# Kernel tuning notes

Measured on AMD Instinct MI355X. Metric: run time of the kernel, lower is better.

The kernel has to match this reference:

```python
import jax, jax.numpy as jnp
import numpy as np

BN_EPS = 1e-5
BN_SCALE = 1.0 / np.sqrt(1.0 + BN_EPS).astype(np.float32)  # running_mean=0, running_var=1


def _conv1x1(x, w, b=None):
    y = jnp.einsum('bchw,oc->bohw', x, w)
    if b is not None:
        y = y + b.reshape(1, -1, 1, 1)
    return y


def _bn(x, g, b):
    # eval-mode BN with running_mean=0, running_var=1
    return x * (BN_SCALE * g).reshape(1, -1, 1, 1) + b.reshape(1, -1, 1, 1)


def _spatial_attn(x, w, b):
    avg = jnp.mean(x, axis=1, keepdims=True)
    mx = jnp.max(x, axis=1, keepdims=True)
    s = jnp.concatenate([avg, mx], axis=1)  # [B,2,H,W]
    y = jax.lax.conv_general_dilated(s, w, (1, 1), [(3, 3), (3, 3)],
                                     dimension_numbers=('NCHW', 'OIHW', 'NCHW'))
    return jax.nn.sigmoid(y + b.reshape(1, -1, 1, 1))  # [B,1,H,W]


def _channel_attn(x, w1, b1, w2, b2):
    avg = jnp.mean(x, axis=(2, 3))  # [B,C]
    mx = jnp.max(x, axis=(2, 3))
    fc = lambda v: jax.nn.relu(v @ w1.T + b1) @ w2.T + b2
    return jax.nn.sigmoid(fc(avg) + fc(mx))[:, :, None, None]  # [B,C,1,1]


def setup_inputs() -> dict:
    key = jax.random.key(0)
    B, C, H, W = 8, 256, 48, 48
    Cr, Cm = C // 8, C // 16
    ks = iter(jax.random.split(key, 24))
    n = lambda shape, scale=0.05: jax.random.normal(next(ks), shape, jnp.float32) * scale
    return dict(
        rgb=jax.random.normal(next(ks), (B, C, H, W), jnp.float32),
        chm=jax.random.normal(next(ks), (B, C, H, W), jnp.float32),
        rgb_sa_w=n((1, 2, 7, 7)), rgb_sa_b=jnp.zeros((1,), jnp.float32),
        chm_sa_w=n((1, 2, 7, 7)), chm_sa_b=jnp.zeros((1,), jnp.float32),
        rgb_fc1_w=n((Cm, C)), rgb_fc1_b=jnp.zeros((Cm,), jnp.float32),
        rgb_fc2_w=n((C, Cm)), rgb_fc2_b=jnp.zeros((C,), jnp.float32),
        chm_fc1_w=n((Cm, C)), chm_fc1_b=jnp.zeros((Cm,), jnp.float32),
        chm_fc2_w=n((C, Cm)), chm_fc2_b=jnp.zeros((C,), jnp.float32),
        rq_w=n((Cr, C)), rq_b=jnp.zeros((Cr,), jnp.float32),
        rk_w=n((Cr, C)), rk_b=jnp.zeros((Cr,), jnp.float32),
        rv_w=n((C, C)), rv_b=jnp.zeros((C,), jnp.float32),
        dq_w=n((Cr, C)), dq_b=jnp.zeros((Cr,), jnp.float32),
        dk_w=n((Cr, C)), dk_b=jnp.zeros((Cr,), jnp.float32),
        dv_w=n((C, C)), dv_b=jnp.zeros((C,), jnp.float32),
        gate_w=n((C, 2 * C)), gate_b=jnp.zeros((C,), jnp.float32),
        mlp1_w=n((24, C)), mlp1_g=jnp.ones((24,), jnp.float32), mlp1_b=jnp.zeros((24,), jnp.float32),
        mlp2_w=n((1, 24)), mlp2_g=jnp.ones((1,), jnp.float32), mlp2_b=jnp.zeros((1,), jnp.float32),
    )


def reference(rgb, chm, rgb_sa_w, rgb_sa_b, chm_sa_w, chm_sa_b,
              rgb_fc1_w, rgb_fc1_b, rgb_fc2_w, rgb_fc2_b,
              chm_fc1_w, chm_fc1_b, chm_fc2_w, chm_fc2_b,
              rq_w, rq_b, rk_w, rk_b, rv_w, rv_b,
              dq_w, dq_b, dk_w, dk_b, dv_w, dv_b,
              gate_w, gate_b, mlp1_w, mlp1_g, mlp1_b, mlp2_w, mlp2_g, mlp2_b):
    B, C, H, W = rgb.shape
    N = H * W
    Cr = rq_w.shape[0]
    scale = Cr ** -0.5

    # channel / spatial attentions
    rgb_sa = _spatial_attn(rgb, rgb_sa_w, rgb_sa_b)
    chm_sa = _spatial_attn(chm, chm_sa_w, chm_sa_b)
    rgb_ca = _channel_attn(rgb, rgb_fc1_w, rgb_fc1_b, rgb_fc2_w, rgb_fc2_b)
    chm_ca = _channel_attn(chm, chm_fc1_w, chm_fc1_b, chm_fc2_w, chm_fc2_b)

    attn_rgb = rgb * chm_sa * chm_ca
    attn_chm = chm * rgb_sa * rgb_ca

    # CAWF dual cross-modal attention
    flat = lambda x: x.reshape(B, -1, N)
    rq = flat(_conv1x1(rgb, rq_w, rq_b))   # [B,Cr,N]
    rk = flat(_conv1x1(rgb, rk_w, rk_b))
    rv = flat(_conv1x1(rgb, rv_w, rv_b))   # [B,C,N]
    dq = flat(_conv1x1(chm, dq_w, dq_b))
    dk = flat(_conv1x1(chm, dk_w, dk_b))
    dv = flat(_conv1x1(chm, dv_w, dv_b))

    rgb_attn = jax.nn.softmax(jnp.einsum('bcn,bcm->bnm', rq, dk) * scale, axis=-1)  # [B,N,N]
    chm_attn = jax.nn.softmax(jnp.einsum('bcn,bcm->bnm', dq, rk) * scale, axis=-1)
    rgb_att = jnp.einsum('bcn,bnm->bcm', rv, rgb_attn).reshape(B, C, H, W)
    chm_att = jnp.einsum('bcn,bnm->bcm', dv, chm_attn).reshape(B, C, H, W)

    c = jnp.concatenate([rgb_att, chm_att], axis=1)
    g = jax.nn.sigmoid(_conv1x1(c, gate_w, gate_b))
    c_fused = rgb_att * g + chm_att * (1.0 - g)
    d_fused = rgb_att * chm_att
    output = c_fused + d_fused

    h = jax.nn.relu(_bn(_conv1x1(output, mlp1_w), mlp1_g, mlp1_b))
    h = jax.nn.sigmoid(_bn(_conv1x1(h, mlp2_w), mlp2_g, mlp2_b))
    weight = jax.nn.sigmoid(h)  # double sigmoid as in original mlp (ConvBNSig + nn.Sigmoid)

    return attn_rgb + attn_chm * weight
```

## Files before the change

### kernel.cpp

```cpp
#include <hip/hip_runtime.h>
#include <hip/hip_bf16.h>
#include <cstdint>

#define DI __device__ __forceinline__

typedef float f32x4 __attribute__((ext_vector_type(4)));
typedef short bf16x8 __attribute__((ext_vector_type(8)));
typedef unsigned short u16x4 __attribute__((ext_vector_type(4)));

constexpr int B_ = 8, C_ = 256, HH = 48, WW = 48, N_ = 2304, CR = 32;
constexpr float QK_SCALE = 0.17677669529663687f;
constexpr float BN_SC = 0.99999500003749968f;

constexpr size_t QK_SZ   = (size_t)B_*N_*CR*2;
constexpr size_t V_SZ    = (size_t)B_*C_*N_*2;
constexpr size_t OFF_RQT = 0;
constexpr size_t OFF_RKT = OFF_RQT + QK_SZ;
constexpr size_t OFF_DQT = OFF_RKT + QK_SZ;
constexpr size_t OFF_DKT = OFF_DQT + QK_SZ;
constexpr size_t OFF_RV  = OFF_DKT + QK_SZ;
constexpr size_t OFF_DV  = OFF_RV + V_SZ;
constexpr size_t OFF_ATT = OFF_DV + V_SZ;
constexpr size_t ATT_SZ  = 2ull*B_*C_*N_*2;
constexpr size_t OFF_FUSED = OFF_RV;
constexpr size_t OFF_SCONV = OFF_ATT + ATT_SZ;
constexpr size_t SCONV_SZ  = 2ull*B_*2*N_*4;
constexpr size_t OFF_SA    = OFF_SCONV + SCONV_SZ;
constexpr size_t SA_SZ     = 2ull*B_*N_*4;
constexpr size_t OFF_CAVG  = OFF_SA + SA_SZ;
constexpr size_t CST_SZ    = 2ull*B_*C_*4;
constexpr size_t OFF_CMAX  = OFF_CAVG + CST_SZ;
constexpr size_t OFF_CA    = OFF_CMAX + CST_SZ;
constexpr size_t OFF_WMAP  = OFF_CA + CST_SZ;
constexpr size_t OFF_WPROJ = OFF_WMAP + (size_t)B_*N_*4;
constexpr size_t WPROJ_SZ  = 2ull*320*256*2;
constexpr size_t OFF_WGATE = OFF_WPROJ + WPROJ_SZ;
constexpr size_t WS_NEEDED = OFF_WGATE + 256ull*512*2;

DI float bf2f(unsigned short u){ union{unsigned int i; float f;} v; v.i = ((unsigned int)u)<<16; return v.f; }
DI unsigned short f2bf(float f){ union{float f; unsigned int i;} v; v.f=f; unsigned int r = v.i + 0x7fffu + ((v.i>>16)&1u); return (unsigned short)(r>>16); }
DI float sigm(float x){ return 1.0f/(1.0f+__expf(-x)); }
DI u16x4 pk4(float p0, float p1, float p2, float p3){
  union { __hip_bfloat162 h[2]; u16x4 v; } u;
  u.h[0] = __float22bfloat162_rn(make_float2(p0, p1));
  u.h[1] = __float22bfloat162_rn(make_float2(p2, p3));
  return u.v;
}

__global__ void k_prep_w(const float* rq_w, const float* rk_w, const float* rv_w,
                         const float* dq_w, const float* dk_w, const float* dv_w,
                         const float* gate_w, unsigned short* wproj, unsigned short* wgate){
  int i = blockIdx.x*256 + threadIdx.x;
  if (i < 163840){
    int mod = i / 81920, r = (i >> 8) % 320, c = i & 255;
    const float* q = mod ? dq_w : rq_w;
    const float* k = mod ? dk_w : rk_w;
    const float* v = mod ? dv_w : rv_w;
    float val = (r < 32) ? q[r*256+c] : (r < 64 ? k[(r-32)*256+c] : v[(r-64)*256+c]);
    wproj[i] = f2bf(val);
  } else {
    int j = i - 163840;
    if (j < 131072) wgate[j] = f2bf(gate_w[j]);
  }
}

__global__ void k_red_spatial(const float* rgb, const float* chm, float* sconv){
  int mod = blockIdx.y;
  const float* X = mod ? chm : rgb;
  int b = blockIdx.x / (N_/64);
  int pix0 = (blockIdx.x % (N_/64)) * 64;
  int p = threadIdx.x & 63, g = threadIdx.x >> 6;
  const float* base = X + (size_t)b*C_*N_ + pix0 + p;
  float s = 0.f, mx = -INFINITY;
  for (int c = g*64; c < g*64+64; ++c){ float v = base[(size_t)c*N_]; s += v; mx = fmaxf(mx, v); }
  __shared__ float ls[4][64], lm[4][64];
  ls[g][p] = s; lm[g][p] = mx;
  __syncthreads();
  if (g == 0){
    s = ls[0][p]+ls[1][p]+ls[2][p]+ls[3][p];
    mx = fmaxf(fmaxf(lm[0][p],lm[1][p]), fmaxf(lm[2][p],lm[3][p]));
    sconv[((size_t)(mod*B_+b)*2 + 0)*N_ + pix0+p] = s*(1.f/256.f);
    sconv[((size_t)(mod*B_+b)*2 + 1)*N_ + pix0+p] = mx;
  }
}

__global__ void k_red_channel(const float* rgb, const float* chm, float* cavg, float* cmax){
  int mod = blockIdx.y;
  const float* X = mod ? chm : rgb;
  int b = blockIdx.x >> 8, c = blockIdx.x & 255;
  const float* base = X + ((size_t)b*C_ + c)*N_;
  float s = 0.f, mx = -INFINITY;
  for (int i = threadIdx.x; i < N_; i += 256){ float v = base[i]; s += v; mx = fmaxf(mx, v); }
  for (int m = 32; m; m >>= 1){ s += __shfl_xor(s, m); mx = fmaxf(mx, __shfl_xor(mx, m)); }
  __shared__ float ss[4], sm[4];
  int w = threadIdx.x >> 6;
  if ((threadIdx.x & 63) == 0){ ss[w] = s; sm[w] = mx; }
  __syncthreads();
  if (threadIdx.x == 0){
    s = ss[0]+ss[1]+ss[2]+ss[3];
    mx = fmaxf(fmaxf(sm[0],sm[1]), fmaxf(sm[2],sm[3]));
    cavg[(mod*B_+b)*C_ + c] = s*(1.f/(float)N_);
    cmax[(mod*B_+b)*C_ + c] = mx;
  }
}

__global__ void k_sa_ca(const float* sconv, const float* rgb_sa_w, const float* rgb_sa_b,
                        const float* chm_sa_w, const float* chm_sa_b, float* sa,
                        const float* cavg, const float* cmax,
                        const float* rw1, const float* rb1, const float* rw2, const float* rb2,
                        const float* cw1, const float* cb1, const float* cw2, const float* cb2,
                        float* ca){
  int x = blockIdx.x;
  if (x < 144){
    int mod = x / 72;
    int idx = (x % 72)*256 + threadIdx.x;
    int b = idx / N_, pix = idx % N_;
    int y = pix / WW, xx0 = pix % WW;
    const float* w7 = mod ? chm_sa_w : rgb_sa_w;
    float acc = (mod ? chm_sa_b : rgb_sa_b)[0];
    const float* sin0 = sconv + (size_t)(mod*B_+b)*2*N_;
    #pragma unroll
    for (int ic = 0; ic < 2; ++ic)
      for (int ky = 0; ky < 7; ++ky){
        int yy = y + ky - 3; if (yy < 0 || yy >= HH) continue;
        for (int kx = 0; kx < 7; ++kx){
          int xx = xx0 + kx - 3; if (xx < 0 || xx >= WW) continue;
          acc += w7[(ic*7+ky)*7+kx] * sin0[ic*N_ + yy*WW + xx];
        }
      }
    sa[(mod*B_+b)*N_ + pix] = sigm(acc);
  } else {
    int y = x - 144;
    int mod = y >> 3, b = y & 7;
    const float* w1 = mod ? cw1 : rw1;  const float* b1 = mod ? cb1 : rb1;
    const float* w2 = mod ? cw2 : rw2;  const float* b2 = mod ? cb2 : rb2;
    __shared__ float va[256], vm[256], h1a[16], h1m[16];
    int t = threadIdx.x;
    va[t] = cavg[(mod*B_+b)*C_ + t];
    vm[t] = cmax[(mod*B_+b)*C_ + t];
    __syncthreads();
    if (t < 32){
      int j = t & 15;
      const float* v = (t >= 16) ? vm : va;
      float s = b1[j];
      for (int c = 0; c < 256; ++c) s += w1[j*256+c]*v[c];
      float* hp = (t >= 16) ? h1m : h1a;
      hp[j] = fmaxf(s, 0.f);
    }
    __syncthreads();
    float fa = b2[t], fm = b2[t];
    #pragma unroll
    for (int j = 0; j < 16; ++j){ fa += w2[t*16+j]*h1a[j]; fm += w2[t*16+j]*h1m[j]; }
    ca[(mod*B_+b)*C_ + t] = sigm(fa + fm);
  }
}

__global__ __launch_bounds__(256, 2) void k_proj(
                       const float* rgb, const float* chm, const unsigned short* wproj,
                       const float* rq_b, const float* rk_b, const float* rv_b,
                       const float* dq_b, const float* dk_b, const float* dv_b,
                       unsigned short* wsu){
  int mod = blockIdx.z, b = blockIdx.y;
  int pix0 = blockIdx.x * 64;
  const float* X = (mod ? chm : rgb) + (size_t)b*C_*N_;
  const unsigned short* Wm = wproj + (size_t)mod*320*256;
  int lane = threadIdx.x & 63, w = threadIdx.x >> 6;
  int l15 = lane & 15, g = lane >> 4;
  __shared__ unsigned short xs[32*68];
  int srow = threadIdx.x >> 3, scol = (threadIdx.x & 7)*8;
  f32x4 acc[5][4];
  #pragma unroll
  for (int i = 0; i < 5; ++i)
    #pragma unroll
    for (int j = 0; j < 4; ++j) acc[i][j] = 0.f;
  for (int k0 = 0; k0 < 256; k0 += 32){
    const float* sp = X + (size_t)(k0 + srow)*N_ + pix0 + scol;
    float4 v0 = *(const float4*)sp;
    float4 v1 = *(const float4*)(sp + 4);
    u16x4 h0 = { f2bf(v0.x), f2bf(v0.y), f2bf(v0.z), f2bf(v0.w) };
    u16x4 h1 = { f2bf(v1.x), f2bf(v1.y), f2bf(v1.z), f2bf(v1.w) };
    __syncthreads();
    *(u16x4*)(xs + srow*68 + scol) = h0;
    *(u16x4*)(xs + srow*68 + scol + 4) = h1;
    __syncthreads();
    bf16x8 af[5];
    #pragma unroll
    for (int cf = 0; cf < 5; ++cf)
      af[cf] = *(const bf16x8*)(Wm + (size_t)(w*80 + cf*16 + l15)*256 + k0 + g*8);
    bf16x8 bx[4];
    #pragma unroll
    for (int mf = 0; mf < 4; ++mf)
      #pragma unroll
      for (int j = 0; j < 8; ++j)
        bx[mf][j] = (short)xs[(g*8+j)*68 + mf*16 + l15];
    #pragma unroll
    for (int cf = 0; cf < 5; ++cf)
      #pragma unroll
      for (int mf = 0; mf < 4; ++mf)
        acc[cf][mf] = __builtin_amdgcn_mfma_f32_16x16x32_bf16(af[cf], bx[mf], acc[cf][mf], 0, 0, 0);
  }
  const float* qb = mod ? dq_b : rq_b;
  const float* kb = mod ? dk_b : rk_b;
  const float* vb = mod ? dv_b : rv_b;
  unsigned short* qT = wsu + (mod ? OFF_DQT : OFF_RQT)/2;
  unsigned short* kT = wsu + (mod ? OFF_DKT : OFF_RKT)/2;
  unsigned short* vB = wsu + (mod ? OFF_DV  : OFF_RV )/2;
  #pragma unroll
  for (int cf = 0; cf < 5; ++cf){
    int base = w*80 + cf*16;
    #pragma unroll
    for (int mf = 0; mf < 4; ++mf){
      int col = pix0 + mf*16 + l15;
      if (base < 32){
        int o4 = base + g*4;
        u16x4 pk = { f2bf(acc[cf][mf][0] + qb[o4]),   f2bf(acc[cf][mf][1] + qb[o4+1]),
                     f2bf(acc[cf][mf][2] + qb[o4+2]), f2bf(acc[cf][mf][3] + qb[o4+3]) };
        *(u16x4*)(qT + (size_t)(b*N_ + col)*32 + o4) = pk;
      } else if (base < 64){
        int o4 = base - 32 + g*4;
        u16x4 pk = { f2bf(acc[cf][mf][0] + kb[o4]),   f2bf(acc[cf][mf][1] + kb[o4+1]),
                     f2bf(acc[cf][mf][2] + kb[o4+2]), f2bf(acc[cf][mf][3] + kb[o4+3]) };
        *(u16x4*)(kT + (size_t)(b*N_ + col)*32 + o4) = pk;
      } else {
        #pragma unroll
        for (int r = 0; r < 4; ++r){
          int o = base - 64 + g*4 + r;
          vB[((size_t)b*C_ + o)*N_ + col] = f2bf(acc[cf][mf][r] + vb[o]);
        }
      }
    }
  }
}

__global__ void k_phase_a(unsigned short* wsu){
  int a = blockIdx.z, b = blockIdx.y;
  int lane = threadIdx.x & 63, w = threadIdx.x >> 6;
  int l15 = lane & 15, g = lane >> 4;
  int nb0 = blockIdx.x*64;
  int n0 = nb0 + w*16;
  const unsigned short* Q = wsu + (a ? OFF_DQT : OFF_RQT)/2;
  const unsigned short* K = wsu + (a ? OFF_RKT : OFF_DKT)/2;
  bf16x8 af = *(const bf16x8*)(Q + (size_t)(b*N_ + n0 + l15)*32 + g*8);
  float lrun[4] = {0.f,0.f,0.f,0.f};
  for (int m0 = 0; m0 < N_; m0 += 64){
    f32x4 d[4];
    #pragma unroll
    for (int s = 0; s < 4; ++s){
      bf16x8 bk = *(const bf16x8*)(K + (size_t)(b*N_ + m0 + s*16 + l15)*32 + g*8);
      f32x4 z = 0.f;
      d[s] = __builtin_amdgcn_mfma_f32_16x16x32_bf16(af, bk, z, 0, 0, 0);
    }
    #pragma unroll
    for (int r = 0; r < 4; ++r)
      lrun[r] += (__expf(d[0][r]*QK_SCALE)+__expf(d[1][r]*QK_SCALE))
               + (__expf(d[2][r]*QK_SCALE)+__expf(d[3][r]*QK_SCALE));
  }
  #pragma unroll
  for (int r = 0; r < 4; ++r)
    #pragma unroll
    for (int msk = 1; msk < 16; msk <<= 1) lrun[r] += __shfl_xor(lrun[r], msk);
  __shared__ float lsv[64];
  if (l15 == 0){
    #pragma unroll
    for (int r = 0; r < 4; ++r) lsv[w*16 + g*4 + r] = 1.0f / lrun[r];
  }
  __syncthreads();
  unsigned short* V = wsu + (a ? OFF_DV : OFF_RV)/2 + ((size_t)b*C_ + threadIdx.x)*N_ + nb0;
  #pragma unroll
  for (int j8 = 0; j8 < 8; ++j8){
    bf16x8 vv = *(const bf16x8*)(V + j8*8);
    bf16x8 ov;
    #pragma unroll
    for (int e = 0; e < 8; ++e)
      ov[e] = (short)f2bf(bf2f((unsigned short)vv[e]) * lsv[j8*8 + e]);
    *(bf16x8*)(V + j8*8) = ov;
  }
}

__global__ __launch_bounds__(256, 3) void k_pv3(
                          const unsigned short* wsu, unsigned short* att){
  int orig = blockIdx.x;
  int logical = (orig & 7)*72 + (orig >> 3);
  int pair = logical / 36, mblk = logical % 36;
  int a = pair >> 3, b = pair & 7;
  int m0 = mblk*64;
  int lane = threadIdx.x & 63, w = threadIdx.x >> 6;
  int l15 = lane & 15, g = lane >> 4;
  int qn = (w >> 1)*32, qm = (w & 1)*32;
  const unsigned short* Q = wsu + (a ? OFF_DQT : OFF_RQT)/2;
  const unsigned short* K = wsu + (a ? OFF_RKT : OFF_DKT)/2;
  const unsigned short* V = wsu + (a ? OFF_DV  : OFF_RV )/2;
  __shared__ __align__(16) unsigned char plds[2][64*128];

  bf16x8 kb[2];
  #pragma unroll
  for (int s = 0; s < 2; ++s)
    kb[s] = *(const bf16x8*)(K + (size_t)(b*N_ + m0 + qm + s*16 + l15)*32 + g*8);

  f32x4 acc[4][4];
  #pragma unroll
  for (int i = 0; i < 4; ++i)
    #pragma unroll
    for (int j = 0; j < 4; ++j) acc[i][j] = 0.f;

  auto computeP = [&](int n0, int buf){
    bf16x8 qa[2];
    #pragma unroll
    for (int fr = 0; fr < 2; ++fr)
      qa[fr] = *(const bf16x8*)(Q + (size_t)(b*N_ + n0 + qn + fr*16 + l15)*32 + g*8);
    #pragma unroll
    for (int fr = 0; fr < 2; ++fr)
      #pragma unroll
      for (int fm = 0; fm < 2; ++fm){
        f32x4 z = 0.f;
        f32x4 d = __builtin_amdgcn_mfma_f32_16x16x32_bf16(qa[fr], kb[fm], z, 0, 0, 0);
        int ml = qm + fm*16 + l15;
        unsigned char* row = plds[buf] + ml*128;
        int sw = (ml & 7) << 4;
        u16x4 pk = pk4(__expf(d[0]*QK_SCALE), __expf(d[1]*QK_SCALE),
                       __expf(d[2]*QK_SCALE), __expf(d[3]*QK_SCALE));
        *(u16x4*)(row + (((qn + fr*16 + g*4)*2) ^ sw)) = pk;
      }
  };

  computeP(0, 0);
  __syncthreads();
  for (int t = 0; t < 36; ++t){
    int n0 = t*64;
    const unsigned char* pbuf = plds[t & 1];
    bf16x8 pb[2][4];
    #pragma unroll
    for (int ks = 0; ks < 2; ++ks)
      #pragma unroll
      for (int mf = 0; mf < 4; ++mf){
        int ml = mf*16 + l15;
        pb[ks][mf] = *(const bf16x8*)(pbuf + ml*128 + (((ks*32 + g*8)*2) ^ ((ml&7)<<4)));
      }
    bf16x8 av[2][4];
    #pragma unroll
    for (int ks = 0; ks < 2; ++ks)
      #pragma unroll
      for (int cf = 0; cf < 4; ++cf)
        av[ks][cf] = *(const bf16x8*)(V + ((size_t)b*C_ + w*64 + cf*16 + l15)*N_ + n0 + ks*32 + g*8);
    if (t < 35) computeP(n0 + 64, (t+1)&1);
    __builtin_amdgcn_s_setprio(1);
    #pragma unroll
    for (int ks = 0; ks < 2; ++ks)
      #pragma unroll
      for (int cf = 0; cf < 4; ++cf)
        #pragma unroll
        for (int mf = 0; mf < 4; ++mf)
          acc[cf][mf] = __builtin_amdgcn_mfma_f32_16x16x32_bf16(av[ks][cf], pb[ks][mf], acc[cf][mf], 0, 0, 0);
    __builtin_amdgcn_s_setprio(0);
    __syncthreads();
  }
  unsigned short* ap = att + (((size_t)a*8 + b)*256)*N_;
  #pragma unroll
  for (int cf = 0; cf < 4; ++cf)
    #pragma unroll
    for (int mf = 0; mf < 4; ++mf)
      #pragma unroll
      for (int r = 0; r < 4; ++r){
        int c = w*64 + cf*16 + g*4 + r;
        int m = m0 + mf*16 + l15;
        ap[(size_t)c*N_ + m] = f2bf(acc[cf][mf][r]);
      }
}

__global__ __launch_bounds__(256, 2) void k_gatefuse(
                           const unsigned short* att, const unsigned short* wgate,
                           const float* gate_b, unsigned short* fused){
  int b = blockIdx.y, m0 = blockIdx.x*32;
  int lane = threadIdx.x & 63, w = threadIdx.x >> 6;
  int l15 = lane & 15, g = lane >> 4;
  __shared__ unsigned short ats[32][520];
  int row8 = threadIdx.x >> 3;
  int mq = (threadIdx.x & 7)*4;
  for (int rb = 0; rb < 16; ++rb){
    int k = rb*32 + row8;
    int aa = k >> 8, c = k & 255;
    size_t base = (((size_t)aa*8 + b)*256 + c)*N_ + m0 + mq;
    u16x4 p0 = *(const u16x4*)(att + base);
    #pragma unroll
    for (int j = 0; j < 4; ++j) ats[mq + j][k] = p0[j];
  }
  __syncthreads();
  f32x4 acc[4][2];
  #pragma unroll
  for (int i = 0; i < 4; ++i){ acc[i][0] = 0.f; acc[i][1] = 0.f; }
  for (int k0 = 0; k0 < 512; k0 += 32){
    bf16x8 aw[4], bt[2];
    #pragma unroll
    for (int of = 0; of < 4; ++of)
      aw[of] = *(const bf16x8*)(wgate + (size_t)(w*64 + of*16 + l15)*512 + k0 + g*8);
    #pragma unroll
    for (int mf = 0; mf < 2; ++mf)
      bt[mf] = *(const bf16x8*)(&ats[mf*16 + l15][k0 + g*8]);
    #pragma unroll
    for (int of = 0; of < 4; ++of)
      #pragma unroll
      for (int mf = 0; mf < 2; ++mf)
        acc[of][mf] = __builtin_amdgcn_mfma_f32_16x16x32_bf16(aw[of], bt[mf], acc[of][mf], 0, 0, 0);
  }
  #pragma unroll
  for (int of = 0; of < 4; ++of){
    int o4 = w*64 + of*16 + g*4;
    float4 gb4 = *(const float4*)(gate_b + o4);
    #pragma unroll
    for (int mf = 0; mf < 2; ++mf){
      int ml = mf*16 + l15;
      int m = m0 + ml;
      u16x4 ra4 = *(const u16x4*)(&ats[ml][o4]);
      u16x4 da4 = *(const u16x4*)(&ats[ml][256 + o4]);
      #pragma unroll
      for (int r = 0; r < 4; ++r){
        float gg = sigm(acc[of][mf][r] + (&gb4.x)[r]);
        float ra = bf2f(ra4[r]);
        float da = bf2f(da4[r]);
        float fv = ra*gg + da*(1.f - gg) + ra*da;
        fused[((size_t)b*C_ + o4 + r)*N_ + m] = f2bf(fv);
      }
    }
  }
}

__global__ void k_mlp(const unsigned short* fused, const float* w1, const float* g1, const float* b1,
                      const float* w2, const float* g2, const float* b2, float* wmap){
  int b = blockIdx.x / 36, pix0 = (blockIdx.x % 36)*64;
  __shared__ unsigned short ft[256*64];
  __shared__ float hs[24][64];
  const unsigned short* F = fused + (size_t)b*C_*N_ + pix0;
  int c0 = threadIdx.x >> 3, l8 = threadIdx.x & 7;
  for (int cc = 0; cc < 256; cc += 32)
    *(bf16x8*)(ft + (size_t)(cc + c0)*64 + l8*8) = *(const bf16x8*)(F + (size_t)(cc + c0)*N_ + l8*8);
  __syncthreads();
  int p = threadIdx.x & 63, jg = threadIdx.x >> 6;
  float h[6] = {0.f,0.f,0.f,0.f,0.f,0.f};
  for (int c = 0; c < 256; ++c){
    float v = bf2f(ft[c*64 + p]);
    #pragma unroll
    for (int jj = 0; jj < 6; ++jj) h[jj] += w1[(jg*6+jj)*256 + c] * v;
  }
  #pragma unroll
  for (int jj = 0; jj < 6; ++jj) hs[jg*6+jj][p] = h[jj];
  __syncthreads();
  if (threadIdx.x < 64){
    int pp = threadIdx.x;
    float s2 = 0.f;
    #pragma unroll
    for (int j = 0; j < 24; ++j){
      float hj = fmaxf(hs[j][pp]*(BN_SC*g1[j]) + b1[j], 0.f);
      s2 += w2[j]*hj;
    }
    s2 = s2*(BN_SC*g2[0]) + b2[0];
    wmap[b*N_ + pix0 + pp] = sigm(sigm(s2));
  }
}

__global__ void k_final(const float* rgb, const float* chm, const float* sa, const float* ca,
                        const float* wmap, float* out){
  const int total4 = B_*C_*N_/4;
  for (int i = blockIdx.x*blockDim.x + threadIdx.x; i < total4; i += gridDim.x*blockDim.x){
    int e = i*4;
    int b = e / (C_*N_);
    int rem = e % (C_*N_);
    int c = rem / N_;
    int pix = rem % N_;
    float4 rv = *(const float4*)(rgb + e);
    float4 cv = *(const float4*)(chm + e);
    float4 sc = *(const float4*)(sa + (size_t)(B_ + b)*N_ + pix);
    float4 sr = *(const float4*)(sa + (size_t)b*N_ + pix);
    float4 wm = *(const float4*)(wmap + (size_t)b*N_ + pix);
    float cac = ca[(B_ + b)*C_ + c];
    float car = ca[b*C_ + c];
    float4 o;
    o.x = rv.x*sc.x*cac + cv.x*sr.x*car*wm.x;
    o.y = rv.y*sc.y*cac + cv.y*sr.y*car*wm.y;
    o.z = rv.z*sc.z*cac + cv.z*sr.z*car*wm.z;
    o.w = rv.w*sc.w*cac + cv.w*sr.w*car*wm.w;
    *(float4*)(out + e) = o;
  }
}

extern "C" void kernel_launch(void* const* d_in, const int* in_sizes, int n_in,
                              void* d_out, int out_size, void* d_ws, size_t ws_size,
                              hipStream_t stream){
  if (ws_size < WS_NEEDED) return;
  const float* rgb      = (const float*)d_in[0];
  const float* chm      = (const float*)d_in[1];
  const float* rgb_sa_w = (const float*)d_in[2];
  const float* rgb_sa_b = (const float*)d_in[3];
  const float* chm_sa_w = (const float*)d_in[4];
  const float* chm_sa_b = (const float*)d_in[5];
  const float* rgb_fc1_w= (const float*)d_in[6];
  const float* rgb_fc1_b= (const float*)d_in[7];
  const float* rgb_fc2_w= (const float*)d_in[8];
  const float* rgb_fc2_b= (const float*)d_in[9];
  const float* chm_fc1_w= (const float*)d_in[10];
  const float* chm_fc1_b= (const float*)d_in[11];
  const float* chm_fc2_w= (const float*)d_in[12];
  const float* chm_fc2_b= (const float*)d_in[13];
  const float* rq_w = (const float*)d_in[14];
  const float* rq_b = (const float*)d_in[15];
  const float* rk_w = (const float*)d_in[16];
  const float* rk_b = (const float*)d_in[17];
  const float* rv_w = (const float*)d_in[18];
  const float* rv_b = (const float*)d_in[19];
  const float* dq_w = (const float*)d_in[20];
  const float* dq_b = (const float*)d_in[21];
  const float* dk_w = (const float*)d_in[22];
  const float* dk_b = (const float*)d_in[23];
  const float* dv_w = (const float*)d_in[24];
  const float* dv_b = (const float*)d_in[25];
  const float* gate_w = (const float*)d_in[26];
  const float* gate_b = (const float*)d_in[27];
  const float* mlp1_w = (const float*)d_in[28];
  const float* mlp1_g = (const float*)d_in[29];
  const float* mlp1_b = (const float*)d_in[30];
  const float* mlp2_w = (const float*)d_in[31];
  const float* mlp2_g = (const float*)d_in[32];
  const float* mlp2_b = (const float*)d_in[33];

  char* ws = (char*)d_ws;
  unsigned short* wsu   = (unsigned short*)d_ws;
  float* sconv = (float*)(ws + OFF_SCONV);
  float* sa    = (float*)(ws + OFF_SA);
  float* cavg  = (float*)(ws + OFF_CAVG);
  float* cmax  = (float*)(ws + OFF_CMAX);
  float* ca    = (float*)(ws + OFF_CA);
  float* wmap  = (float*)(ws + OFF_WMAP);
  unsigned short* wproj = (unsigned short*)(ws + OFF_WPROJ);
  unsigned short* wgate = (unsigned short*)(ws + OFF_WGATE);
  unsigned short* att   = (unsigned short*)(ws + OFF_ATT);
  unsigned short* fused = (unsigned short*)(ws + OFF_FUSED);

  k_prep_w<<<dim3(1152), dim3(256), 0, stream>>>(rq_w, rk_w, rv_w, dq_w, dk_w, dv_w, gate_w, wproj, wgate);
  k_red_spatial<<<dim3(288,2), dim3(256), 0, stream>>>(rgb, chm, sconv);
  k_red_channel<<<dim3(2048,2), dim3(256), 0, stream>>>(rgb, chm, cavg, cmax);
  k_sa_ca<<<dim3(160), dim3(256), 0, stream>>>(sconv, rgb_sa_w, rgb_sa_b, chm_sa_w, chm_sa_b, sa,
                                               cavg, cmax, rgb_fc1_w, rgb_fc1_b, rgb_fc2_w, rgb_fc2_b,
                                               chm_fc1_w, chm_fc1_b, chm_fc2_w, chm_fc2_b, ca);
  k_proj<<<dim3(36,8,2), dim3(256), 0, stream>>>(rgb, chm, wproj, rq_b, rk_b, rv_b, dq_b, dk_b, dv_b, wsu);
  k_phase_a<<<dim3(36,8,2), dim3(256), 0, stream>>>(wsu);
  k_pv3<<<dim3(576), dim3(256), 0, stream>>>(wsu, att);
  k_gatefuse<<<dim3(72,8), dim3(256), 0, stream>>>(att, wgate, gate_b, fused);
  k_mlp<<<dim3(288), dim3(256), 0, stream>>>(fused, mlp1_w, mlp1_g, mlp1_b, mlp2_w, mlp2_g, mlp2_b, wmap);
  k_final<<<dim3(2048), dim3(256), 0, stream>>>(rgb, chm, sa, ca, wmap, (float*)d_out);
}
```

Before: 312.3 us.

## Fuse spatial and channel reductions; restructure PV kernel to skip LDS staging

The spatial and channel reductions are merged into one kernel that stages 128-channel by 64-pixel tiles in shared memory and emits per-tile channel partials, followed by a small combine kernel. This removes the second full read of both inputs. The PV attention kernel now has each wave recompute the full 64-wide P tile in registers and feed it directly to 16x16x16 MFMAs, dropping the LDS double buffer and the per-iteration barrier. The cost is redundant QK/exp work across the four waves. Block indices are remapped so phase_a and pv interleave batches across CUs.

```diff
diff --git a/kernel.cpp b/kernel.cpp
--- a/kernel.cpp
+++ b/kernel.cpp
@@ -6,6 +6,7 @@
 
 typedef float f32x4 __attribute__((ext_vector_type(4)));
 typedef short bf16x8 __attribute__((ext_vector_type(8)));
+typedef short bf16x4 __attribute__((ext_vector_type(4)));
 typedef unsigned short u16x4 __attribute__((ext_vector_type(4)));
 
 constexpr int B_ = 8, C_ = 256, HH = 48, WW = 48, N_ = 2304, CR = 32;
@@ -22,6 +23,8 @@
 constexpr size_t OFF_DV  = OFF_RV + V_SZ;
 constexpr size_t OFF_ATT = OFF_DV + V_SZ;
 constexpr size_t ATT_SZ  = 2ull*B_*C_*N_*2;
+constexpr size_t OFF_PCS = OFF_ATT;
+constexpr size_t OFF_PCM = OFF_ATT + 2ull*8*36*256*4;
 constexpr size_t OFF_FUSED = OFF_RV;
 constexpr size_t OFF_SCONV = OFF_ATT + ATT_SZ;
 constexpr size_t SCONV_SZ  = 2ull*B_*2*N_*4;
@@ -40,12 +43,6 @@
 DI float bf2f(unsigned short u){ union{unsigned int i; float f;} v; v.i = ((unsigned int)u)<<16; return v.f; }
 DI unsigned short f2bf(float f){ union{float f; unsigned int i;} v; v.f=f; unsigned int r = v.i + 0x7fffu + ((v.i>>16)&1u); return (unsigned short)(r>>16); }
 DI float sigm(float x){ return 1.0f/(1.0f+__expf(-x)); }
-DI u16x4 pk4(float p0, float p1, float p2, float p3){
-  union { __hip_bfloat162 h[2]; u16x4 v; } u;
-  u.h[0] = __float22bfloat162_rn(make_float2(p0, p1));
-  u.h[1] = __float22bfloat162_rn(make_float2(p2, p3));
-  return u.v;
-}
 
 __global__ void k_prep_w(const float* rq_w, const float* rk_w, const float* rv_w,
                          const float* dq_w, const float* dk_w, const float* dv_w,
@@ -64,19 +61,48 @@
   }
 }
 
-__global__ void k_red_spatial(const float* rgb, const float* chm, float* sconv){
+__global__ __launch_bounds__(256, 2) void k_redfuse(const float* rgb, const float* chm,
+                                                    float* sconv, float* pcs, float* pcm){
   int mod = blockIdx.y;
-  const float* X = mod ? chm : rgb;
-  int b = blockIdx.x / (N_/64);
-  int pix0 = (blockIdx.x % (N_/64)) * 64;
-  int p = threadIdx.x & 63, g = threadIdx.x >> 6;
-  const float* base = X + (size_t)b*C_*N_ + pix0 + p;
+  int b = blockIdx.x / 36, nt = blockIdx.x % 36;
+  int pix0 = nt*64;
+  const float* X = (mod ? chm : rgb) + (size_t)b*C_*N_ + pix0;
+  __shared__ float xt[128][65];
+  __shared__ float ls[4][64], lm[4][64];
+  int t = threadIdx.x;
+  int p = t & 63, cg = t >> 6;
+  int srow0 = t >> 4, scol = (t & 15)*4;
   float s = 0.f, mx = -INFINITY;
-  for (int c = g*64; c < g*64+64; ++c){ float v = base[(size_t)c*N_]; s += v; mx = fmaxf(mx, v); }
-  __shared__ float ls[4][64], lm[4][64];
-  ls[g][p] = s; lm[g][p] = mx;
+  float* pcsb = pcs + ((size_t)(mod*8+b)*36 + nt)*256;
+  float* pcmb = pcm + ((size_t)(mod*8+b)*36 + nt)*256;
+  for (int half = 0; half < 2; ++half){
+    __syncthreads();
+    #pragma unroll
+    for (int rr = 0; rr < 8; ++rr){
+      int row = rr*16 + srow0;
+      float4 v = *(const float4*)(X + (size_t)(half*128 + row)*N_ + scol);
+      xt[row][scol] = v.x; xt[row][scol+1] = v.y; xt[row][scol+2] = v.z; xt[row][scol+3] = v.w;
+    }
+    __syncthreads();
+    #pragma unroll 8
+    for (int cc = 0; cc < 32; ++cc){
+      float v = xt[cg*32 + cc][p];
+      s += v; mx = fmaxf(mx, v);
+    }
+    if (t < 128){
+      float cs = 0.f, cm = -INFINITY;
+      #pragma unroll 8
+      for (int pp = 0; pp < 64; ++pp){
+        float v = xt[t][pp];
+        cs += v; cm = fmaxf(cm, v);
+      }
+      pcsb[half*128 + t] = cs;
+      pcmb[half*128 + t] = cm;
+    }
+  }
+  ls[cg][p] = s; lm[cg][p] = mx;
   __syncthreads();
-  if (g == 0){
+  if (cg == 0){
     s = ls[0][p]+ls[1][p]+ls[2][p]+ls[3][p];
     mx = fmaxf(fmaxf(lm[0][p],lm[1][p]), fmaxf(lm[2][p],lm[3][p]));
     sconv[((size_t)(mod*B_+b)*2 + 0)*N_ + pix0+p] = s*(1.f/256.f);
@@ -84,24 +110,15 @@
   }
 }
 
-__global__ void k_red_channel(const float* rgb, const float* chm, float* cavg, float* cmax){
-  int mod = blockIdx.y;
-  const float* X = mod ? chm : rgb;
-  int b = blockIdx.x >> 8, c = blockIdx.x & 255;
-  const float* base = X + ((size_t)b*C_ + c)*N_;
+__global__ void k_red_combine(const float* pcs, const float* pcm, float* cavg, float* cmax){
+  int mod = blockIdx.x >> 3, b = blockIdx.x & 7, c = threadIdx.x;
   float s = 0.f, mx = -INFINITY;
-  for (int i = threadIdx.x; i < N_; i += 256){ float v = base[i]; s += v; mx = fmaxf(mx, v); }
-  for (int m = 32; m; m >>= 1){ s += __shfl_xor(s, m); mx = fmaxf(mx, __shfl_xor(mx, m)); }
-  __shared__ float ss[4], sm[4];
-  int w = threadIdx.x >> 6;
-  if ((threadIdx.x & 63) == 0){ ss[w] = s; sm[w] = mx; }
-  __syncthreads();
-  if (threadIdx.x == 0){
-    s = ss[0]+ss[1]+ss[2]+ss[3];
-    mx = fmaxf(fmaxf(sm[0],sm[1]), fmaxf(sm[2],sm[3]));
-    cavg[(mod*B_+b)*C_ + c] = s*(1.f/(float)N_);
-    cmax[(mod*B_+b)*C_ + c] = mx;
-  }
+  for (int nt = 0; nt < 36; ++nt){
+    s += pcs[((size_t)(mod*8+b)*36 + nt)*256 + c];
+    mx = fmaxf(mx, pcm[((size_t)(mod*8+b)*36 + nt)*256 + c]);
+  }
+  cavg[(mod*B_+b)*C_ + c] = s*(1.f/(float)N_);
+  cmax[(mod*B_+b)*C_ + c] = mx;
 }
 
 __global__ void k_sa_ca(const float* sconv, const float* rgb_sa_w, const float* rgb_sa_b,
@@ -233,10 +250,13 @@
 }
 
 __global__ void k_phase_a(unsigned short* wsu){
-  int a = blockIdx.z, b = blockIdx.y;
+  int orig = blockIdx.x;
+  int b = orig & 7;
+  int logical = orig >> 3;
+  int a = logical / 36;
+  int nb0 = (logical % 36)*64;
   int lane = threadIdx.x & 63, w = threadIdx.x >> 6;
   int l15 = lane & 15, g = lane >> 4;
-  int nb0 = blockIdx.x*64;
   int n0 = nb0 + w*16;
   const unsigned short* Q = wsu + (a ? OFF_DQT : OFF_RQT)/2;
   const unsigned short* K = wsu + (a ? OFF_RKT : OFF_DKT)/2;
@@ -277,25 +297,22 @@
   }
 }
 
-__global__ __launch_bounds__(256, 3) void k_pv3(
-                          const unsigned short* wsu, unsigned short* att){
+__global__ __launch_bounds__(256, 3) void k_pv4(const unsigned short* wsu, unsigned short* att){
   int orig = blockIdx.x;
-  int logical = (orig & 7)*72 + (orig >> 3);
-  int pair = logical / 36, mblk = logical % 36;
-  int a = pair >> 3, b = pair & 7;
+  int b = orig & 7;
+  int logical = orig >> 3;
+  int a = logical / 36, mblk = logical % 36;
   int m0 = mblk*64;
   int lane = threadIdx.x & 63, w = threadIdx.x >> 6;
   int l15 = lane & 15, g = lane >> 4;
-  int qn = (w >> 1)*32, qm = (w & 1)*32;
   const unsigned short* Q = wsu + (a ? OFF_DQT : OFF_RQT)/2;
   const unsigned short* K = wsu + (a ? OFF_RKT : OFF_DKT)/2;
   const unsigned short* V = wsu + (a ? OFF_DV  : OFF_RV )/2;
-  __shared__ __align__(16) unsigned char plds[2][64*128];
-
-  bf16x8 kb[2];
-  #pragma unroll
-  for (int s = 0; s < 2; ++s)
-    kb[s] = *(const bf16x8*)(K + (size_t)(b*N_ + m0 + qm + s*16 + l15)*32 + g*8);
+
+  bf16x8 kb[4];
+  #pragma unroll
+  for (int mt = 0; mt < 4; ++mt)
+    kb[mt] = *(const bf16x8*)(K + (size_t)(b*N_ + m0 + mt*16 + l15)*32 + g*8);
 
   f32x4 acc[4][4];
   #pragma unroll
@@ -303,67 +320,62 @@
     #pragma unroll
     for (int j = 0; j < 4; ++j) acc[i][j] = 0.f;
 
-  auto computeP = [&](int n0, int buf){
-    bf16x8 qa[2];
-    #pragma unroll
-    for (int fr = 0; fr < 2; ++fr)
-      qa[fr] = *(const bf16x8*)(Q + (size_t)(b*N_ + n0 + qn + fr*16 + l15)*32 + g*8);
-    #pragma unroll
-    for (int fr = 0; fr < 2; ++fr)
-      #pragma unroll
-      for (int fm = 0; fm < 2; ++fm){
-        f32x4 z = 0.f;
-        f32x4 d = __builtin_amdgcn_mfma_f32_16x16x32_bf16(qa[fr], kb[fm], z, 0, 0, 0);
-        int ml = qm + fm*16 + l15;
-        unsigned char* row = plds[buf] + ml*128;
-        int sw = (ml & 7) << 4;
-        u16x4 pk = pk4(__expf(d[0]*QK_SCALE), __expf(d[1]*QK_SCALE),
-                       __expf(d[2]*QK_SCALE), __expf(d[3]*QK_SCALE));
-        *(u16x4*)(row + (((qn + fr*16 + g*4)*2) ^ sw)) = pk;
-      }
-  };
-
-  computeP(0, 0);
-  __syncthreads();
-  for (int t = 0; t < 36; ++t){
-    int n0 = t*64;
-    const unsigned char* pbuf = plds[t & 1];
-    bf16x8 pb[2][4];
-    #pragma unroll
-    for (int ks = 0; ks < 2; ++ks)
-      #pragma unroll
-      for (int mf = 0; mf < 4; ++mf){
-        int ml = mf*16 + l15;
-        pb[ks][mf] = *(const bf16x8*)(pbuf + ml*128 + (((ks*32 + g*8)*2) ^ ((ml&7)<<4)));
-      }
-    bf16x8 av[2][4];
-    #pragma unroll
-    for (int ks = 0; ks < 2; ++ks)
+  const unsigned short* Qrow = Q + (size_t)(b*N_ + l15)*32 + g*8;
+  const unsigned short* Vrow = V + ((size_t)b*C_ + w*64 + l15)*N_ + g*4;
+
+  bf16x8 qa = *(const bf16x8*)Qrow;
+  bf16x4 av[4];
+  #pragma unroll
+  for (int cf = 0; cf < 4; ++cf)
+    av[cf] = *(const bf16x4*)(Vrow + (size_t)cf*16*N_);
+
+  #pragma unroll 2
+  for (int t = 0; t < 144; ++t){
+    int n0 = t*16;
+    bf16x8 qa_n; bf16x4 av_n[4];
+    if (t < 143){
+      qa_n = *(const bf16x8*)(Qrow + (size_t)(n0+16)*32);
       #pragma unroll
       for (int cf = 0; cf < 4; ++cf)
-        av[ks][cf] = *(const bf16x8*)(V + ((size_t)b*C_ + w*64 + cf*16 + l15)*N_ + n0 + ks*32 + g*8);
-    if (t < 35) computeP(n0 + 64, (t+1)&1);
+        av_n[cf] = *(const bf16x4*)(Vrow + (size_t)cf*16*N_ + n0 + 16);
+    }
+    f32x4 d[4];
+    #pragma unroll
+    for (int mt = 0; mt < 4; ++mt){
+      f32x4 z = 0.f;
+      d[mt] = __builtin_amdgcn_mfma_f32_16x16x32_bf16(qa, kb[mt], z, 0, 0, 0);
+    }
+    bf16x4 pb[4];
+    #pragma unroll
+    for (int mt = 0; mt < 4; ++mt){
+      union { __hip_bfloat162 h[2]; bf16x4 v; } u;
+      u.h[0] = __float22bfloat162_rn(make_float2(__expf(d[mt][0]*QK_SCALE), __expf(d[mt][1]*QK_SCALE)));
+      u.h[1] = __float22bfloat162_rn(make_float2(__expf(d[mt][2]*QK_SCALE), __expf(d[mt][3]*QK_SCALE)));
+      pb[mt] = u.v;
+    }
     __builtin_amdgcn_s_setprio(1);
     #pragma unroll
-    for (int ks = 0; ks < 2; ++ks)
-      #pragma unroll
-      for (int cf = 0; cf < 4; ++cf)
-        #pragma unroll
-        for (int mf = 0; mf < 4; ++mf)
-          acc[cf][mf] = __builtin_amdgcn_mfma_f32_16x16x32_bf16(av[ks][cf], pb[ks][mf], acc[cf][mf], 0, 0, 0);
+    for (int cf = 0; cf < 4; ++cf)
+      #pragma unroll
+      for (int mt = 0; mt < 4; ++mt)
+        acc[cf][mt] = __builtin_amdgcn_mfma_f32_16x16x16bf16_1k(av[cf], pb[mt], acc[cf][mt], 0, 0, 0);
     __builtin_amdgcn_s_setprio(0);
-    __syncthreads();
+    if (t < 143){
+      qa = qa_n;
+      #pragma unroll
+      for (int cf = 0; cf < 4; ++cf) av[cf] = av_n[cf];
+    }
   }
   unsigned short* ap = att + (((size_t)a*8 + b)*256)*N_;
   #pragma unroll
   for (int cf = 0; cf < 4; ++cf)
     #pragma unroll
-    for (int mf = 0; mf < 4; ++mf)
+    for (int mt = 0; mt < 4; ++mt)
       #pragma unroll
       for (int r = 0; r < 4; ++r){
         int c = w*64 + cf*16 + g*4 + r;
-        int m = m0 + mf*16 + l15;
-        ap[(size_t)c*N_ + m] = f2bf(acc[cf][mf][r]);
+        int m = m0 + mt*16 + l15;
+        ap[(size_t)c*N_ + m] = f2bf(acc[cf][mt][r]);
       }
 }
 
@@ -529,20 +541,22 @@
   float* cmax  = (float*)(ws + OFF_CMAX);
   float* ca    = (float*)(ws + OFF_CA);
   float* wmap  = (float*)(ws + OFF_WMAP);
+  float* pcs   = (float*)(ws + OFF_PCS);
+  float* pcm   = (float*)(ws + OFF_PCM);
   unsigned short* wproj = (unsigned short*)(ws + OFF_WPROJ);
   unsigned short* wgate = (unsigned short*)(ws + OFF_WGATE);
   unsigned short* att   = (unsigned short*)(ws + OFF_ATT);
   unsigned short* fused = (unsigned short*)(ws + OFF_FUSED);
 
   k_prep_w<<<dim3(1152), dim3(256), 0, stream>>>(rq_w, rk_w, rv_w, dq_w, dk_w, dv_w, gate_w, wproj, wgate);
-  k_red_spatial<<<dim3(288,2), dim3(256), 0, stream>>>(rgb, chm, sconv);
-  k_red_channel<<<dim3(2048,2), dim3(256), 0, stream>>>(rgb, chm, cavg, cmax);
+  k_redfuse<<<dim3(288,2), dim3(256), 0, stream>>>(rgb, chm, sconv, pcs, pcm);
+  k_red_combine<<<dim3(16), dim3(256), 0, stream>>>(pcs, pcm, cavg, cmax);
   k_sa_ca<<<dim3(160), dim3(256), 0, stream>>>(sconv, rgb_sa_w, rgb_sa_b, chm_sa_w, chm_sa_b, sa,
                                                cavg, cmax, rgb_fc1_w, rgb_fc1_b, rgb_fc2_w, rgb_fc2_b,
                                                chm_fc1_w, chm_fc1_b, chm_fc2_w, chm_fc2_b, ca);
   k_proj<<<dim3(36,8,2), dim3(256), 0, stream>>>(rgb, chm, wproj, rq_b, rk_b, rv_b, dq_b, dk_b, dv_b, wsu);
-  k_phase_a<<<dim3(36,8,2), dim3(256), 0, stream>>>(wsu);
-  k_pv3<<<dim3(576), dim3(256), 0, stream>>>(wsu, att);
+  k_phase_a<<<dim3(576), dim3(256), 0, stream>>>(wsu);
+  k_pv4<<<dim3(576), dim3(256), 0, stream>>>(wsu, att);
   k_gatefuse<<<dim3(72,8), dim3(256), 0, stream>>>(att, wgate, gate_b, fused);
   k_mlp<<<dim3(288), dim3(256), 0, stream>>>(fused, mlp1_w, mlp1_g, mlp1_b, mlp2_w, mlp2_g, mlp2_b, wmap);
   k_final<<<dim3(2048), dim3(256), 0, stream>>>(rgb, chm, sa, ca, wmap, (float*)d_out);
```

New measurement: 385.6 us. 1.23x slower.
